# Kernel tuning notes

Measured on AMD Instinct MI355X. Metric: run time of the kernel, lower is better.

Reference implementation:

```python
import jax, jax.numpy as jnp
import numpy as np

EPS = 1e-5
N, E, G = 65536, 262144, 256
DV, DE, DG = 256, 128, 256


def _ln(x):
    # LayerNorm without affine over the last dim
    mu = jnp.mean(x, axis=-1, keepdims=True)
    var = jnp.mean(jnp.square(x - mu), axis=-1, keepdims=True)
    return (x - mu) * jax.lax.rsqrt(var + EPS)


def setup_inputs() -> dict:
    key = jax.random.key(0)
    ks = jax.random.split(key, 14)
    inp = {
        'fv': jax.random.normal(ks[0], (N, DV), jnp.float32),
        'fe': jax.random.normal(ks[1], (E, DE), jnp.float32),
        'fg': jax.random.normal(ks[2], (G, DG), jnp.float32),
        'fv_pos': jax.random.normal(ks[3], (N, 3), jnp.float32),
        'fv_c': jax.random.normal(ks[4], (N, DV), jnp.float32),
        'fe_c': jax.random.normal(ks[5], (E, DE), jnp.float32),
        'fv_pos_c': jax.random.normal(ks[6], (N, DV), jnp.float32),
        # learned params (original zero-inits the modulation Linears; we use
        # small random weights so the kernel path is exercised)
        'W_v': jax.random.normal(ks[7], (2 * DV, DV), jnp.float32) * 0.02,
        'b_v': jnp.zeros((2 * DV,), jnp.float32),
        'W_vpos': jax.random.normal(ks[8], (DE, DV), jnp.float32) * 0.02,
        'b_vpos': jnp.zeros((DE,), jnp.float32),
        'W_e': jax.random.normal(ks[9], (2 * DE, DE), jnp.float32) * 0.02,
        'b_e': jnp.zeros((2 * DE,), jnp.float32),
        'g_gamma': jnp.ones((DG,), jnp.float32),
        'g_beta': jnp.zeros((DG,), jnp.float32),
        'W_pos': jax.random.normal(ks[10], (1, DG), jnp.float32) * 0.02,
        'b_pos': jnp.zeros((1,), jnp.float32),
        'src': jax.random.randint(ks[11], (E,), 0, N, jnp.int32),
        'dst': jax.random.randint(ks[12], (E,), 0, N, jnp.int32),
        'node_gid': (jnp.arange(N, dtype=jnp.int32) // (N // G)),
    }
    return inp


def reference(fv, fe, fg, fv_pos, fv_c, fe_c, fv_pos_c,
              W_v, b_v, W_vpos, b_vpos, W_e, b_e,
              g_gamma, g_beta, W_pos, b_pos,
              src, dst, node_gid):
    act = jax.nn.silu
    # --- node modulation ---
    mod_v = act(fv_c + fv_pos_c) @ W_v.T + b_v            # [N, 2*DV]
    shift_v, scale_v = jnp.split(mod_v, 2, axis=1)
    fv_out = _ln(fv) * (1.0 + scale_v) + shift_v
    # --- edge modulation with gsddmm('add') gather ---
    fvp = fv_pos_c @ W_vpos.T + b_vpos                    # [N, DE]
    fv2e = fvp[src] + fvp[dst]                            # sddmm add [E, DE]
    mod_e = act(fe_c + fv2e) @ W_e.T + b_e                # [E, 2*DE]
    shift_e, scale_e = jnp.split(mod_e, 2, axis=1)
    fe_out = _ln(fe) * (1.0 + scale_e) + shift_e
    # --- adaptive position scale-norm (per-graph, equivariant) ---
    ones = jnp.ones((N,), fv_pos.dtype)
    cnt = jax.ops.segment_sum(ones, node_gid, num_segments=G)          # [G]
    mean = jax.ops.segment_sum(fv_pos, node_gid, num_segments=G) / cnt[:, None]
    centered = fv_pos - mean[node_gid]                                  # [N, 3]
    sq = jax.ops.segment_sum(jnp.sum(jnp.square(centered), axis=1), node_gid, num_segments=G)
    rms = jnp.sqrt(sq / (cnt * 3.0) + EPS)                              # [G]
    pos_n = centered / rms[node_gid][:, None]
    s = act(fg) @ W_pos.T + b_pos                                       # [G, 1]
    fv_pos_out = pos_n * (1.0 + s)[node_gid]
    # --- graph LayerNorm (affine) ---
    fg_out = _ln(fg) * g_gamma + g_beta
    return (fv_out, fe_out, fg_out, fv_pos_out)
```

## Files before the change

### kernel.cpp

```cpp
#include <hip/hip_runtime.h>

#define N_NODES 65536
#define N_EDGES 262144
#define N_GRAPH 256
#define DV 256
#define DE 128
#define DG 256
#define EPS 1e-5f

typedef __bf16 bf16_t;
typedef bf16_t bf16x8 __attribute__((ext_vector_type(8)));
typedef float f32x4 __attribute__((ext_vector_type(4)));
typedef unsigned short ushort_t;

__device__ __forceinline__ float silu_f(float x) {
  return x / (1.0f + __expf(-x));
}
__device__ __forceinline__ unsigned short f2bf(float f) {
  unsigned int u = __float_as_uint(f);
  u += 0x7fffu + ((u >> 16) & 1u);
  return (unsigned short)(u >> 16);
}
__device__ __forceinline__ float bf2f(unsigned short h) {
  return __uint_as_float(((unsigned int)h) << 16);
}
__device__ __forceinline__ void split_bf(float x, ushort_t& hi, ushort_t& lo) {
  hi = f2bf(x);
  lo = f2bf(x - bf2f(hi));
}
__device__ __forceinline__ void wave_reduce2(float& s1, float& s2) {
  #pragma unroll
  for (int off = 32; off > 0; off >>= 1) {
    s1 += __shfl_xor(s1, off);
    s2 += __shfl_xor(s2, off);
  }
}

__global__ __launch_bounds__(256) void k_prep(
    const float* __restrict__ W_v, const float* __restrict__ W_e,
    const float* __restrict__ W_vpos, ushort_t* __restrict__ Wv_bf,
    ushort_t* __restrict__ We_bf, ushort_t* __restrict__ Wvpos_bf) {
  int idx = blockIdx.x * 256 + threadIdx.x;
  const float* s;
  ushort_t* d;
  int o;
  if (idx < 32768) { s = W_v; d = Wv_bf; o = idx; }
  else if (idx < 40960) { s = W_e; d = We_bf; o = idx - 32768; }
  else { s = W_vpos; d = Wvpos_bf; o = idx - 40960; }
  float4 v = *(const float4*)&s[(size_t)o * 4];
  ushort4 r;
  r.x = f2bf(v.x); r.y = f2bf(v.y); r.z = f2bf(v.z); r.w = f2bf(v.w);
  *(ushort4*)&d[(size_t)o * 4] = r;
}

__global__ __launch_bounds__(512) void k_fvp(
    const float* __restrict__ fv_pos_c, const ushort_t* __restrict__ Wvpos_bf,
    const float* __restrict__ b_vpos, float* __restrict__ fvp) {
  __shared__ __align__(16) ushort_t Xh[32][264];
  __shared__ __align__(16) ushort_t Xl[32][264];
  const int tid = threadIdx.x;
  const int l = tid & 63, w = tid >> 6;
  const int m0 = blockIdx.x * 32;
  #pragma unroll
  for (int i = 0; i < 4; ++i) {
    int idx = i * 512 + tid;
    int r = idx >> 6, c4 = idx & 63;
    float4 v = *(const float4*)&fv_pos_c[(size_t)(m0 + r) * DV + c4 * 4];
    ushort4 h, lo;
    split_bf(v.x, h.x, lo.x);
    split_bf(v.y, h.y, lo.y);
    split_bf(v.z, h.z, lo.z);
    split_bf(v.w, h.w, lo.w);
    *(ushort4*)&Xh[r][c4 * 4] = h;
    *(ushort4*)&Xl[r][c4 * 4] = lo;
  }
  __syncthreads();
  f32x4 acc[2];
  acc[0] = (f32x4)(0.f);
  acc[1] = (f32x4)(0.f);
  const int mrow = (w & 1) * 16;
  const int ncol0 = (w >> 1) * 32;
  const int arow = mrow + (l & 15);
  for (int kc = 0; kc < 8; ++kc) {
    int ke = kc * 32 + (l >> 4) * 8;
    bf16x8 ah = *(const bf16x8*)&Xh[arow][ke];
    bf16x8 al = *(const bf16x8*)&Xl[arow][ke];
    #pragma unroll
    for (int ni = 0; ni < 2; ++ni) {
      bf16x8 b = *(const bf16x8*)&Wvpos_bf[(size_t)(ncol0 + ni * 16 + (l & 15)) * DV + ke];
      acc[ni] = __builtin_amdgcn_mfma_f32_16x16x32_bf16(al, b, acc[ni], 0, 0, 0);
      acc[ni] = __builtin_amdgcn_mfma_f32_16x16x32_bf16(ah, b, acc[ni], 0, 0, 0);
    }
  }
  #pragma unroll
  for (int ni = 0; ni < 2; ++ni) {
    int col = ncol0 + ni * 16 + (l & 15);
    float bias = b_vpos[col];
    #pragma unroll
    for (int j = 0; j < 4; ++j) {
      int row = m0 + mrow + (l >> 4) * 4 + j;
      fvp[(size_t)row * DE + col] = acc[ni][j] + bias;
    }
  }
}

__global__ __launch_bounds__(512) void k_node(
    const float* __restrict__ fv, const float* __restrict__ fv_c,
    const float* __restrict__ fv_pos_c, const ushort_t* __restrict__ Wv_bf,
    const float* __restrict__ b_v, float* __restrict__ fv_out) {
  __shared__ __align__(16) ushort_t Xh[32][264];
  __shared__ __align__(16) ushort_t Xl[32][264];
  __shared__ float muL[32], rsL[32];
  const int tid = threadIdx.x;
  const int l = tid & 63, w = tid >> 6;
  const int m0 = blockIdx.x * 32;
  #pragma unroll
  for (int rr = 0; rr < 4; ++rr) {
    int row = w * 4 + rr;
    float4 v = *(const float4*)&fv[(size_t)(m0 + row) * DV + l * 4];
    float s1 = v.x + v.y + v.z + v.w;
    float s2 = v.x * v.x + v.y * v.y + v.z * v.z + v.w * v.w;
    wave_reduce2(s1, s2);
    if (l == 0) {
      float mu = s1 * (1.0f / DV);
      float var = s2 * (1.0f / DV) - mu * mu;
      muL[row] = mu;
      rsL[row] = rsqrtf(var + EPS);
    }
  }
  #pragma unroll
  for (int i = 0; i < 4; ++i) {
    int idx = i * 512 + tid;
    int r = idx >> 6, c4 = idx & 63;
    size_t g = (size_t)(m0 + r) * DV + c4 * 4;
    float4 a = *(const float4*)&fv_c[g];
    float4 b = *(const float4*)&fv_pos_c[g];
    ushort4 h, lo;
    split_bf(silu_f(a.x + b.x), h.x, lo.x);
    split_bf(silu_f(a.y + b.y), h.y, lo.y);
    split_bf(silu_f(a.z + b.z), h.z, lo.z);
    split_bf(silu_f(a.w + b.w), h.w, lo.w);
    *(ushort4*)&Xh[r][c4 * 4] = h;
    *(ushort4*)&Xl[r][c4 * 4] = lo;
  }
  __syncthreads();
  f32x4 acc[2][4];
  #pragma unroll
  for (int mi = 0; mi < 2; ++mi)
    #pragma unroll
    for (int ni = 0; ni < 4; ++ni) acc[mi][ni] = (f32x4)(0.f);
  int ncol[4];
  ncol[0] = w * 32;
  ncol[1] = w * 32 + 16;
  ncol[2] = DV + w * 32;
  ncol[3] = DV + w * 32 + 16;
  for (int kc = 0; kc < 8; ++kc) {
    int ke = kc * 32 + (l >> 4) * 8;
    bf16x8 ah[2], al[2];
    #pragma unroll
    for (int mi = 0; mi < 2; ++mi) {
      ah[mi] = *(const bf16x8*)&Xh[mi * 16 + (l & 15)][ke];
      al[mi] = *(const bf16x8*)&Xl[mi * 16 + (l & 15)][ke];
    }
    #pragma unroll
    for (int ni = 0; ni < 4; ++ni) {
      bf16x8 b = *(const bf16x8*)&Wv_bf[(size_t)(ncol[ni] + (l & 15)) * DV + ke];
      #pragma unroll
      for (int mi = 0; mi < 2; ++mi) {
        acc[mi][ni] = __builtin_amdgcn_mfma_f32_16x16x32_bf16(al[mi], b, acc[mi][ni], 0, 0, 0);
        acc[mi][ni] = __builtin_amdgcn_mfma_f32_16x16x32_bf16(ah[mi], b, acc[mi][ni], 0, 0, 0);
      }
    }
  }
  #pragma unroll
  for (int ni2 = 0; ni2 < 2; ++ni2) {
    int c = w * 32 + ni2 * 16 + (l & 15);
    float bsh = b_v[c];
    float bsc = b_v[DV + c];
    #pragma unroll
    for (int mi = 0; mi < 2; ++mi)
      #pragma unroll
      for (int j = 0; j < 4; ++j) {
        int row = mi * 16 + (l >> 4) * 4 + j;
        size_t g = (size_t)(m0 + row) * DV + c;
        float v = fv[g];
        float sh = acc[mi][ni2][j] + bsh;
        float sc = acc[mi][ni2 + 2][j] + bsc;
        fv_out[g] = (v - muL[row]) * rsL[row] * (1.0f + sc) + sh;
      }
  }
}

__global__ __launch_bounds__(512) void k_edge(
    const float* __restrict__ fe, const float* __restrict__ fe_c,
    const float* __restrict__ fvp, const int* __restrict__ src,
    const int* __restrict__ dst, const ushort_t* __restrict__ We_bf,
    const float* __restrict__ b_e, float* __restrict__ fe_out) {
  __shared__ __align__(16) ushort_t Xh[64][136];
  __shared__ __align__(16) ushort_t Xl[64][136];
  __shared__ int ss[64], dd[64];
  __shared__ float muL[64], rsL[64];
  const int tid = threadIdx.x;
  const int l = tid & 63, w = tid >> 6;
  const int m0 = blockIdx.x * 64;
  if (tid < 64) ss[tid] = src[m0 + tid];
  else if (tid < 128) dd[tid - 64] = dst[m0 + tid - 64];
  #pragma unroll
  for (int rr = 0; rr < 8; ++rr) {
    int row = w * 8 + rr;
    float2 v = *(const float2*)&fe[(size_t)(m0 + row) * DE + l * 2];
    float s1 = v.x + v.y;
    float s2 = v.x * v.x + v.y * v.y;
    wave_reduce2(s1, s2);
    if (l == 0) {
      float mu = s1 * (1.0f / DE);
      float var = s2 * (1.0f / DE) - mu * mu;
      muL[row] = mu;
      rsL[row] = rsqrtf(var + EPS);
    }
  }
  __syncthreads();
  #pragma unroll
  for (int i = 0; i < 4; ++i) {
    int idx = i * 512 + tid;
    int r = idx >> 5, c4 = idx & 31;
    float4 a = *(const float4*)&fe_c[(size_t)(m0 + r) * DE + c4 * 4];
    float4 p = *(const float4*)&fvp[(size_t)ss[r] * DE + c4 * 4];
    float4 q = *(const float4*)&fvp[(size_t)dd[r] * DE + c4 * 4];
    ushort4 h, lo;
    split_bf(silu_f(a.x + p.x + q.x), h.x, lo.x);
    split_bf(silu_f(a.y + p.y + q.y), h.y, lo.y);
    split_bf(silu_f(a.z + p.z + q.z), h.z, lo.z);
    split_bf(silu_f(a.w + p.w + q.w), h.w, lo.w);
    *(ushort4*)&Xh[r][c4 * 4] = h;
    *(ushort4*)&Xl[r][c4 * 4] = lo;
  }
  __syncthreads();
  f32x4 acc[4][2];
  #pragma unroll
  for (int mi = 0; mi < 4; ++mi) {
    acc[mi][0] = (f32x4)(0.f);
    acc[mi][1] = (f32x4)(0.f);
  }
  for (int kc = 0; kc < 4; ++kc) {
    int ke = kc * 32 + (l >> 4) * 8;
    bf16x8 ah[4], al[4];
    #pragma unroll
    for (int mi = 0; mi < 4; ++mi) {
      ah[mi] = *(const bf16x8*)&Xh[mi * 16 + (l & 15)][ke];
      al[mi] = *(const bf16x8*)&Xl[mi * 16 + (l & 15)][ke];
    }
    #pragma unroll
    for (int ni = 0; ni < 2; ++ni) {
      bf16x8 b = *(const bf16x8*)&We_bf[(size_t)(ni * DE + w * 16 + (l & 15)) * DE + ke];
      #pragma unroll
      for (int mi = 0; mi < 4; ++mi) {
        acc[mi][ni] = __builtin_amdgcn_mfma_f32_16x16x32_bf16(al[mi], b, acc[mi][ni], 0, 0, 0);
        acc[mi][ni] = __builtin_amdgcn_mfma_f32_16x16x32_bf16(ah[mi], b, acc[mi][ni], 0, 0, 0);
      }
    }
  }
  {
    int c = w * 16 + (l & 15);
    float bsh = b_e[c];
    float bsc = b_e[DE + c];
    #pragma unroll
    for (int mi = 0; mi < 4; ++mi)
      #pragma unroll
      for (int j = 0; j < 4; ++j) {
        int row = mi * 16 + (l >> 4) * 4 + j;
        size_t g = (size_t)(m0 + row) * DE + c;
        float v = fe[g];
        float sh = acc[mi][0][j] + bsh;
        float sc = acc[mi][1][j] + bsc;
        fe_out[g] = (v - muL[row]) * rsL[row] * (1.0f + sc) + sh;
      }
  }
}

__global__ __launch_bounds__(256) void k_fg(
    const float* __restrict__ fg, const float* __restrict__ g_gamma,
    const float* __restrict__ g_beta, const float* __restrict__ W_pos,
    const float* __restrict__ b_pos, float* __restrict__ fg_out,
    float* __restrict__ g_s) {
  const int g = blockIdx.x, c = threadIdx.x;
  const int lane = c & 63, wave = c >> 6;
  float x = fg[g * DG + c];
  float sv = silu_f(x) * W_pos[c];
  float s1 = x, s2 = x * x, s3 = sv;
  #pragma unroll
  for (int off = 32; off > 0; off >>= 1) {
    s1 += __shfl_xor(s1, off);
    s2 += __shfl_xor(s2, off);
    s3 += __shfl_xor(s3, off);
  }
  __shared__ float p1[4], p2[4], p3[4];
  if (lane == 0) { p1[wave] = s1; p2[wave] = s2; p3[wave] = s3; }
  __syncthreads();
  s1 = p1[0] + p1[1] + p1[2] + p1[3];
  s2 = p2[0] + p2[1] + p2[2] + p2[3];
  float mu = s1 * (1.0f / DG);
  float var = s2 * (1.0f / DG) - mu * mu;
  float rstd = rsqrtf(var + EPS);
  fg_out[g * DG + c] = (x - mu) * rstd * g_gamma[c] + g_beta[c];
  if (c == 0) g_s[g] = (p3[0] + p3[1] + p3[2] + p3[3]) + b_pos[0];
}

__global__ __launch_bounds__(256) void k_pos_stat(
    const float* __restrict__ fv_pos, const int* __restrict__ gid_arr,
    float* __restrict__ g_stat) {
  const int i = blockIdx.x * 256 + threadIdx.x;
  const int gid = gid_arr[i];
  float x = fv_pos[3 * i + 0];
  float y = fv_pos[3 * i + 1];
  float z = fv_pos[3 * i + 2];
  float q = x * x + y * y + z * z;
  __shared__ int g0s;
  if (threadIdx.x == 0) g0s = gid;
  __syncthreads();
  int g0 = g0s;
  if (__syncthreads_and(gid == g0)) {
    #pragma unroll
    for (int off = 32; off > 0; off >>= 1) {
      x += __shfl_xor(x, off);
      y += __shfl_xor(y, off);
      z += __shfl_xor(z, off);
      q += __shfl_xor(q, off);
    }
    __shared__ float px[4], py[4], pz[4], pq[4];
    const int lane = threadIdx.x & 63, wave = threadIdx.x >> 6;
    if (lane == 0) { px[wave] = x; py[wave] = y; pz[wave] = z; pq[wave] = q; }
    __syncthreads();
    if (threadIdx.x == 0) {
      atomicAdd(&g_stat[g0 * 8 + 0], px[0] + px[1] + px[2] + px[3]);
      atomicAdd(&g_stat[g0 * 8 + 1], py[0] + py[1] + py[2] + py[3]);
      atomicAdd(&g_stat[g0 * 8 + 2], pz[0] + pz[1] + pz[2] + pz[3]);
      atomicAdd(&g_stat[g0 * 8 + 3], pq[0] + pq[1] + pq[2] + pq[3]);
      atomicAdd(&g_stat[g0 * 8 + 4], 256.0f);
    }
  } else {
    atomicAdd(&g_stat[gid * 8 + 0], x);
    atomicAdd(&g_stat[gid * 8 + 1], y);
    atomicAdd(&g_stat[gid * 8 + 2], z);
    atomicAdd(&g_stat[gid * 8 + 3], q);
    atomicAdd(&g_stat[gid * 8 + 4], 1.0f);
  }
}

__global__ __launch_bounds__(256) void k_pos_fin(
    const float* __restrict__ g_stat, const float* __restrict__ g_s,
    float* __restrict__ g_ms) {
  const int g = threadIdx.x;
  float cnt = fmaxf(g_stat[g * 8 + 4], 1.0f);
  float ic = 1.0f / cnt;
  float mx = g_stat[g * 8 + 0] * ic;
  float my = g_stat[g * 8 + 1] * ic;
  float mz = g_stat[g * 8 + 2] * ic;
  float sq = g_stat[g * 8 + 3] - cnt * (mx * mx + my * my + mz * mz);
  sq = fmaxf(sq, 0.0f);
  float rms = sqrtf(sq / (cnt * 3.0f) + EPS);
  g_ms[g * 4 + 0] = mx;
  g_ms[g * 4 + 1] = my;
  g_ms[g * 4 + 2] = mz;
  g_ms[g * 4 + 3] = (1.0f + g_s[g]) / rms;
}

__global__ __launch_bounds__(256) void k_pos_out(
    const float* __restrict__ fv_pos, const int* __restrict__ gid_arr,
    const float* __restrict__ g_ms, float* __restrict__ pos_out) {
  const int i = blockIdx.x * 256 + threadIdx.x;
  const int gid = gid_arr[i];
  float4 ms = *(const float4*)&g_ms[gid * 4];
  pos_out[3 * i + 0] = (fv_pos[3 * i + 0] - ms.x) * ms.w;
  pos_out[3 * i + 1] = (fv_pos[3 * i + 1] - ms.y) * ms.w;
  pos_out[3 * i + 2] = (fv_pos[3 * i + 2] - ms.z) * ms.w;
}

extern "C" void kernel_launch(void* const* d_in, const int* in_sizes, int n_in,
                              void* d_out, int out_size, void* d_ws,
                              size_t ws_size, hipStream_t stream) {
  const float* fv = (const float*)d_in[0];
  const float* fe = (const float*)d_in[1];
  const float* fg = (const float*)d_in[2];
  const float* fv_pos = (const float*)d_in[3];
  const float* fv_c = (const float*)d_in[4];
  const float* fe_c = (const float*)d_in[5];
  const float* fv_pos_c = (const float*)d_in[6];
  const float* W_v = (const float*)d_in[7];
  const float* b_v = (const float*)d_in[8];
  const float* W_vpos = (const float*)d_in[9];
  const float* b_vpos = (const float*)d_in[10];
  const float* W_e = (const float*)d_in[11];
  const float* b_e = (const float*)d_in[12];
  const float* g_gamma = (const float*)d_in[13];
  const float* g_beta = (const float*)d_in[14];
  const float* W_pos = (const float*)d_in[15];
  const float* b_pos = (const float*)d_in[16];
  const int* src = (const int*)d_in[17];
  const int* dst = (const int*)d_in[18];
  const int* node_gid = (const int*)d_in[19];

  float* out = (float*)d_out;
  float* fv_out = out;
  float* fe_out = fv_out + (size_t)N_NODES * DV;
  float* fg_out = fe_out + (size_t)N_EDGES * DE;
  float* pos_out = fg_out + (size_t)N_GRAPH * DG;

  char* ws = (char*)d_ws;
  float* fvp = (float*)ws;
  ushort_t* Wv_bf = (ushort_t*)(ws + 33554432);
  ushort_t* We_bf = (ushort_t*)(ws + 33554432 + 262144);
  ushort_t* Wvpos_bf = (ushort_t*)(ws + 33554432 + 262144 + 65536);
  float* g_stat = (float*)(ws + 33554432 + 262144 + 65536 + 65536);
  float* g_ms = (float*)((char*)g_stat + 8192);
  float* g_s = (float*)((char*)g_ms + 4096);

  hipMemsetAsync(g_stat, 0, 8192, stream);
  k_prep<<<192, 256, 0, stream>>>(W_v, W_e, W_vpos, Wv_bf, We_bf, Wvpos_bf);
  k_fvp<<<N_NODES / 32, 512, 0, stream>>>(fv_pos_c, Wvpos_bf, b_vpos, fvp);
  k_node<<<N_NODES / 32, 512, 0, stream>>>(fv, fv_c, fv_pos_c, Wv_bf, b_v, fv_out);
  k_edge<<<N_EDGES / 64, 512, 0, stream>>>(fe, fe_c, fvp, src, dst, We_bf,
                                           b_e, fe_out);
  k_fg<<<N_GRAPH, 256, 0, stream>>>(fg, g_gamma, g_beta, W_pos, b_pos, fg_out, g_s);
  k_pos_stat<<<N_NODES / 256, 256, 0, stream>>>(fv_pos, node_gid, g_stat);
  k_pos_fin<<<1, 256, 0, stream>>>(g_stat, g_s, g_ms);
  k_pos_out<<<N_NODES / 256, 256, 0, stream>>>(fv_pos, node_gid, g_ms, pos_out);
}
```

Measured before the change: 324.3 us.

## Store fvp in bf16, reorder loads, fuse graph norm with per-graph position norm

The intermediate node projection fvp is now stored as bf16 instead of fp32, halving the bytes written and gathered per edge. k_edge and k_node are reordered so the gather and silu loads are issued before the LayerNorm statistics, and one __syncthreads is removed from k_edge. The four position kernels, the memset and the atomics are folded into one per-graph kernel that assumes each block of 256 nodes belongs to a single graph. A slow full-scan fallback covers other layouts. The bf16 fvp adds rounding error to the edge modulation, and the fast path depends on the sorted, equal-size node_gid layout that the test inputs use.

```diff
diff --git a/kernel.cpp b/kernel.cpp
--- a/kernel.cpp
+++ b/kernel.cpp
@@ -55,7 +55,7 @@
 
 __global__ __launch_bounds__(512) void k_fvp(
     const float* __restrict__ fv_pos_c, const ushort_t* __restrict__ Wvpos_bf,
-    const float* __restrict__ b_vpos, float* __restrict__ fvp) {
+    const float* __restrict__ b_vpos, ushort_t* __restrict__ fvp_bf) {
   __shared__ __align__(16) ushort_t Xh[32][264];
   __shared__ __align__(16) ushort_t Xl[32][264];
   const int tid = threadIdx.x;
@@ -99,7 +99,7 @@
     #pragma unroll
     for (int j = 0; j < 4; ++j) {
       int row = m0 + mrow + (l >> 4) * 4 + j;
-      fvp[(size_t)row * DE + col] = acc[ni][j] + bias;
+      fvp_bf[(size_t)row * DE + col] = f2bf(acc[ni][j] + bias);
     }
   }
 }
@@ -114,20 +114,6 @@
   const int tid = threadIdx.x;
   const int l = tid & 63, w = tid >> 6;
   const int m0 = blockIdx.x * 32;
-  #pragma unroll
-  for (int rr = 0; rr < 4; ++rr) {
-    int row = w * 4 + rr;
-    float4 v = *(const float4*)&fv[(size_t)(m0 + row) * DV + l * 4];
-    float s1 = v.x + v.y + v.z + v.w;
-    float s2 = v.x * v.x + v.y * v.y + v.z * v.z + v.w * v.w;
-    wave_reduce2(s1, s2);
-    if (l == 0) {
-      float mu = s1 * (1.0f / DV);
-      float var = s2 * (1.0f / DV) - mu * mu;
-      muL[row] = mu;
-      rsL[row] = rsqrtf(var + EPS);
-    }
-  }
   #pragma unroll
   for (int i = 0; i < 4; ++i) {
     int idx = i * 512 + tid;
@@ -143,6 +129,20 @@
     *(ushort4*)&Xh[r][c4 * 4] = h;
     *(ushort4*)&Xl[r][c4 * 4] = lo;
   }
+  #pragma unroll
+  for (int rr = 0; rr < 4; ++rr) {
+    int row = w * 4 + rr;
+    float4 v = *(const float4*)&fv[(size_t)(m0 + row) * DV + l * 4];
+    float s1 = v.x + v.y + v.z + v.w;
+    float s2 = v.x * v.x + v.y * v.y + v.z * v.z + v.w * v.w;
+    wave_reduce2(s1, s2);
+    if (l == 0) {
+      float mu = s1 * (1.0f / DV);
+      float var = s2 * (1.0f / DV) - mu * mu;
+      muL[row] = mu;
+      rsL[row] = rsqrtf(var + EPS);
+    }
+  }
   __syncthreads();
   f32x4 acc[2][4];
   #pragma unroll
@@ -193,18 +193,31 @@
 
 __global__ __launch_bounds__(512) void k_edge(
     const float* __restrict__ fe, const float* __restrict__ fe_c,
-    const float* __restrict__ fvp, const int* __restrict__ src,
+    const ushort_t* __restrict__ fvp_bf, const int* __restrict__ src,
     const int* __restrict__ dst, const ushort_t* __restrict__ We_bf,
     const float* __restrict__ b_e, float* __restrict__ fe_out) {
   __shared__ __align__(16) ushort_t Xh[64][136];
   __shared__ __align__(16) ushort_t Xl[64][136];
-  __shared__ int ss[64], dd[64];
   __shared__ float muL[64], rsL[64];
   const int tid = threadIdx.x;
   const int l = tid & 63, w = tid >> 6;
   const int m0 = blockIdx.x * 64;
-  if (tid < 64) ss[tid] = src[m0 + tid];
-  else if (tid < 128) dd[tid - 64] = dst[m0 + tid - 64];
+  #pragma unroll
+  for (int i = 0; i < 4; ++i) {
+    int idx = i * 512 + tid;
+    int r = idx >> 5, c4 = idx & 31;
+    int sr = src[m0 + r], dr = dst[m0 + r];
+    float4 a = *(const float4*)&fe_c[(size_t)(m0 + r) * DE + c4 * 4];
+    ushort4 p = *(const ushort4*)&fvp_bf[(size_t)sr * DE + c4 * 4];
+    ushort4 q = *(const ushort4*)&fvp_bf[(size_t)dr * DE + c4 * 4];
+    ushort4 h, lo;
+    split_bf(silu_f(a.x + bf2f(p.x) + bf2f(q.x)), h.x, lo.x);
+    split_bf(silu_f(a.y + bf2f(p.y) + bf2f(q.y)), h.y, lo.y);
+    split_bf(silu_f(a.z + bf2f(p.z) + bf2f(q.z)), h.z, lo.z);
+    split_bf(silu_f(a.w + bf2f(p.w) + bf2f(q.w)), h.w, lo.w);
+    *(ushort4*)&Xh[r][c4 * 4] = h;
+    *(ushort4*)&Xl[r][c4 * 4] = lo;
+  }
   #pragma unroll
   for (int rr = 0; rr < 8; ++rr) {
     int row = w * 8 + rr;
@@ -220,22 +233,6 @@
     }
   }
   __syncthreads();
-  #pragma unroll
-  for (int i = 0; i < 4; ++i) {
-    int idx = i * 512 + tid;
-    int r = idx >> 5, c4 = idx & 31;
-    float4 a = *(const float4*)&fe_c[(size_t)(m0 + r) * DE + c4 * 4];
-    float4 p = *(const float4*)&fvp[(size_t)ss[r] * DE + c4 * 4];
-    float4 q = *(const float4*)&fvp[(size_t)dd[r] * DE + c4 * 4];
-    ushort4 h, lo;
-    split_bf(silu_f(a.x + p.x + q.x), h.x, lo.x);
-    split_bf(silu_f(a.y + p.y + q.y), h.y, lo.y);
-    split_bf(silu_f(a.z + p.z + q.z), h.z, lo.z);
-    split_bf(silu_f(a.w + p.w + q.w), h.w, lo.w);
-    *(ushort4*)&Xh[r][c4 * 4] = h;
-    *(ushort4*)&Xl[r][c4 * 4] = lo;
-  }
-  __syncthreads();
   f32x4 acc[4][2];
   #pragma unroll
   for (int mi = 0; mi < 4; ++mi) {
@@ -278,15 +275,18 @@
   }
 }
 
-__global__ __launch_bounds__(256) void k_fg(
+__global__ __launch_bounds__(256) void k_fg_pos(
     const float* __restrict__ fg, const float* __restrict__ g_gamma,
     const float* __restrict__ g_beta, const float* __restrict__ W_pos,
-    const float* __restrict__ b_pos, float* __restrict__ fg_out,
-    float* __restrict__ g_s) {
-  const int g = blockIdx.x, c = threadIdx.x;
-  const int lane = c & 63, wave = c >> 6;
-  float x = fg[g * DG + c];
-  float sv = silu_f(x) * W_pos[c];
+    const float* __restrict__ b_pos, const float* __restrict__ fv_pos,
+    const int* __restrict__ node_gid, float* __restrict__ fg_out,
+    float* __restrict__ pos_out) {
+  const int g = blockIdx.x, t = threadIdx.x;
+  const int lane = t & 63, wave = t >> 6;
+  __shared__ float p1[4], p2[4], p3[4];
+  __shared__ float px[4], py[4], pz[4], pq[4];
+  float x = fg[g * DG + t];
+  float sv = silu_f(x) * W_pos[t];
   float s1 = x, s2 = x * x, s3 = sv;
   #pragma unroll
   for (int off = 32; off > 0; off >>= 1) {
@@ -294,7 +294,6 @@
     s2 += __shfl_xor(s2, off);
     s3 += __shfl_xor(s3, off);
   }
-  __shared__ float p1[4], p2[4], p3[4];
   if (lane == 0) { p1[wave] = s1; p2[wave] = s2; p3[wave] = s3; }
   __syncthreads();
   s1 = p1[0] + p1[1] + p1[2] + p1[3];
@@ -302,78 +301,59 @@
   float mu = s1 * (1.0f / DG);
   float var = s2 * (1.0f / DG) - mu * mu;
   float rstd = rsqrtf(var + EPS);
-  fg_out[g * DG + c] = (x - mu) * rstd * g_gamma[c] + g_beta[c];
-  if (c == 0) g_s[g] = (p3[0] + p3[1] + p3[2] + p3[3]) + b_pos[0];
-}
-
-__global__ __launch_bounds__(256) void k_pos_stat(
-    const float* __restrict__ fv_pos, const int* __restrict__ gid_arr,
-    float* __restrict__ g_stat) {
-  const int i = blockIdx.x * 256 + threadIdx.x;
-  const int gid = gid_arr[i];
-  float x = fv_pos[3 * i + 0];
-  float y = fv_pos[3 * i + 1];
-  float z = fv_pos[3 * i + 2];
-  float q = x * x + y * y + z * z;
-  __shared__ int g0s;
-  if (threadIdx.x == 0) g0s = gid;
-  __syncthreads();
-  int g0 = g0s;
-  if (__syncthreads_and(gid == g0)) {
+  fg_out[g * DG + t] = (x - mu) * rstd * g_gamma[t] + g_beta[t];
+  float s_own = (p3[0] + p3[1] + p3[2] + p3[3]) + b_pos[0];
+  const int i = g * 256 + t;
+  const int gid = node_gid[i];
+  float vx = fv_pos[3 * i + 0];
+  float vy = fv_pos[3 * i + 1];
+  float vz = fv_pos[3 * i + 2];
+  if (__syncthreads_and(gid == g)) {
+    float rx = vx, ry = vy, rz = vz, rq = vx * vx + vy * vy + vz * vz;
     #pragma unroll
     for (int off = 32; off > 0; off >>= 1) {
-      x += __shfl_xor(x, off);
-      y += __shfl_xor(y, off);
-      z += __shfl_xor(z, off);
-      q += __shfl_xor(q, off);
-    }
-    __shared__ float px[4], py[4], pz[4], pq[4];
-    const int lane = threadIdx.x & 63, wave = threadIdx.x >> 6;
-    if (lane == 0) { px[wave] = x; py[wave] = y; pz[wave] = z; pq[wave] = q; }
+      rx += __shfl_xor(rx, off);
+      ry += __shfl_xor(ry, off);
+      rz += __shfl_xor(rz, off);
+      rq += __shfl_xor(rq, off);
+    }
+    if (lane == 0) { px[wave] = rx; py[wave] = ry; pz[wave] = rz; pq[wave] = rq; }
     __syncthreads();
-    if (threadIdx.x == 0) {
-      atomicAdd(&g_stat[g0 * 8 + 0], px[0] + px[1] + px[2] + px[3]);
-      atomicAdd(&g_stat[g0 * 8 + 1], py[0] + py[1] + py[2] + py[3]);
-      atomicAdd(&g_stat[g0 * 8 + 2], pz[0] + pz[1] + pz[2] + pz[3]);
-      atomicAdd(&g_stat[g0 * 8 + 3], pq[0] + pq[1] + pq[2] + pq[3]);
-      atomicAdd(&g_stat[g0 * 8 + 4], 256.0f);
-    }
+    float sx = px[0] + px[1] + px[2] + px[3];
+    float sy = py[0] + py[1] + py[2] + py[3];
+    float sz = pz[0] + pz[1] + pz[2] + pz[3];
+    float sq = pq[0] + pq[1] + pq[2] + pq[3];
+    float ic = 1.0f / 256.0f;
+    float mx = sx * ic, my = sy * ic, mz = sz * ic;
+    float cq = fmaxf(sq - 256.0f * (mx * mx + my * my + mz * mz), 0.0f);
+    float rms = sqrtf(cq / (256.0f * 3.0f) + EPS);
+    float sc = (1.0f + s_own) / rms;
+    pos_out[3 * i + 0] = (vx - mx) * sc;
+    pos_out[3 * i + 1] = (vy - my) * sc;
+    pos_out[3 * i + 2] = (vz - mz) * sc;
   } else {
-    atomicAdd(&g_stat[gid * 8 + 0], x);
-    atomicAdd(&g_stat[gid * 8 + 1], y);
-    atomicAdd(&g_stat[gid * 8 + 2], z);
-    atomicAdd(&g_stat[gid * 8 + 3], q);
-    atomicAdd(&g_stat[gid * 8 + 4], 1.0f);
-  }
-}
-
-__global__ __launch_bounds__(256) void k_pos_fin(
-    const float* __restrict__ g_stat, const float* __restrict__ g_s,
-    float* __restrict__ g_ms) {
-  const int g = threadIdx.x;
-  float cnt = fmaxf(g_stat[g * 8 + 4], 1.0f);
-  float ic = 1.0f / cnt;
-  float mx = g_stat[g * 8 + 0] * ic;
-  float my = g_stat[g * 8 + 1] * ic;
-  float mz = g_stat[g * 8 + 2] * ic;
-  float sq = g_stat[g * 8 + 3] - cnt * (mx * mx + my * my + mz * mz);
-  sq = fmaxf(sq, 0.0f);
-  float rms = sqrtf(sq / (cnt * 3.0f) + EPS);
-  g_ms[g * 4 + 0] = mx;
-  g_ms[g * 4 + 1] = my;
-  g_ms[g * 4 + 2] = mz;
-  g_ms[g * 4 + 3] = (1.0f + g_s[g]) / rms;
-}
-
-__global__ __launch_bounds__(256) void k_pos_out(
-    const float* __restrict__ fv_pos, const int* __restrict__ gid_arr,
-    const float* __restrict__ g_ms, float* __restrict__ pos_out) {
-  const int i = blockIdx.x * 256 + threadIdx.x;
-  const int gid = gid_arr[i];
-  float4 ms = *(const float4*)&g_ms[gid * 4];
-  pos_out[3 * i + 0] = (fv_pos[3 * i + 0] - ms.x) * ms.w;
-  pos_out[3 * i + 1] = (fv_pos[3 * i + 1] - ms.y) * ms.w;
-  pos_out[3 * i + 2] = (fv_pos[3 * i + 2] - ms.z) * ms.w;
+    float sx = 0.f, sy = 0.f, sz = 0.f, sq = 0.f, cnt = 0.f;
+    for (int j = 0; j < N_NODES; ++j) {
+      if (node_gid[j] == gid) {
+        float ax = fv_pos[3 * j + 0];
+        float ay = fv_pos[3 * j + 1];
+        float az = fv_pos[3 * j + 2];
+        sx += ax; sy += ay; sz += az;
+        sq += ax * ax + ay * ay + az * az;
+        cnt += 1.0f;
+      }
+    }
+    float ic = 1.0f / fmaxf(cnt, 1.0f);
+    float mx = sx * ic, my = sy * ic, mz = sz * ic;
+    float cq = fmaxf(sq - cnt * (mx * mx + my * my + mz * mz), 0.0f);
+    float rms = sqrtf(cq / (cnt * 3.0f) + EPS);
+    float sg = 0.f;
+    for (int c = 0; c < DG; ++c) sg += silu_f(fg[gid * DG + c]) * W_pos[c];
+    float sc = (1.0f + sg + b_pos[0]) / rms;
+    pos_out[3 * i + 0] = (vx - mx) * sc;
+    pos_out[3 * i + 1] = (vy - my) * sc;
+    pos_out[3 * i + 2] = (vz - mz) * sc;
+  }
 }
 
 extern "C" void kernel_launch(void* const* d_in, const int* in_sizes, int n_in,
@@ -407,22 +387,16 @@
   float* pos_out = fg_out + (size_t)N_GRAPH * DG;
 
   char* ws = (char*)d_ws;
-  float* fvp = (float*)ws;
-  ushort_t* Wv_bf = (ushort_t*)(ws + 33554432);
-  ushort_t* We_bf = (ushort_t*)(ws + 33554432 + 262144);
-  ushort_t* Wvpos_bf = (ushort_t*)(ws + 33554432 + 262144 + 65536);
-  float* g_stat = (float*)(ws + 33554432 + 262144 + 65536 + 65536);
-  float* g_ms = (float*)((char*)g_stat + 8192);
-  float* g_s = (float*)((char*)g_ms + 4096);
-
-  hipMemsetAsync(g_stat, 0, 8192, stream);
+  ushort_t* fvp_bf = (ushort_t*)ws;
+  ushort_t* Wv_bf = (ushort_t*)(ws + 16777216);
+  ushort_t* We_bf = (ushort_t*)(ws + 16777216 + 262144);
+  ushort_t* Wvpos_bf = (ushort_t*)(ws + 16777216 + 262144 + 65536);
+
   k_prep<<<192, 256, 0, stream>>>(W_v, W_e, W_vpos, Wv_bf, We_bf, Wvpos_bf);
-  k_fvp<<<N_NODES / 32, 512, 0, stream>>>(fv_pos_c, Wvpos_bf, b_vpos, fvp);
+  k_fvp<<<N_NODES / 32, 512, 0, stream>>>(fv_pos_c, Wvpos_bf, b_vpos, fvp_bf);
   k_node<<<N_NODES / 32, 512, 0, stream>>>(fv, fv_c, fv_pos_c, Wv_bf, b_v, fv_out);
-  k_edge<<<N_EDGES / 64, 512, 0, stream>>>(fe, fe_c, fvp, src, dst, We_bf,
+  k_edge<<<N_EDGES / 64, 512, 0, stream>>>(fe, fe_c, fvp_bf, src, dst, We_bf,
                                            b_e, fe_out);
-  k_fg<<<N_GRAPH, 256, 0, stream>>>(fg, g_gamma, g_beta, W_pos, b_pos, fg_out, g_s);
-  k_pos_stat<<<N_NODES / 256, 256, 0, stream>>>(fv_pos, node_gid, g_stat);
-  k_pos_fin<<<1, 256, 0, stream>>>(g_stat, g_s, g_ms);
-  k_pos_out<<<N_NODES / 256, 256, 0, stream>>>(fv_pos, node_gid, g_ms, pos_out);
-}
+  k_fg_pos<<<N_GRAPH, 256, 0, stream>>>(fg, g_gamma, g_beta, W_pos, b_pos,
+                                        fv_pos, node_gid, fg_out, pos_out);
+}
```

Result: faster. 301.7 us (-7.0%).
